# Kernel tuning notes

Hardware: AMD Instinct MI355X
Metric: run time of the kernel (lower is better)

## Reference

```python
import jax, jax.numpy as jnp
import numpy as np

N, E, T, F_IN, D, H, C, OUT = 50000, 500000, 8, 128, 256, 32, 8, 64
EPS = 1e-5


def setup_inputs() -> dict:
    key = jax.random.key(0)
    ks = jax.random.split(key, 20)
    p = lambda k, shp, s=0.05: (jax.random.normal(k, shp, jnp.float32) * s)
    feats = jax.random.normal(ks[0], (T, N, F_IN), jnp.float32)
    edge_index = jax.random.randint(ks[1], (T, 2, E), 0, N)
    return dict(
        feats=feats, edge_index=edge_index,
        W1=p(ks[2], (D, F_IN)), a_s1=p(ks[3], (H, C)), a_d1=p(ks[4], (H, C)), b1=jnp.zeros((D,), jnp.float32),
        W2=p(ks[5], (D, D)), a_s2=p(ks[6], (H, C)), a_d2=p(ks[7], (H, C)), b2=jnp.zeros((D,), jnp.float32),
        ln_g=jnp.ones((D,), jnp.float32), ln_b=jnp.zeros((D,), jnp.float32),
        Wqkv=p(ks[8], (3 * D, D)), bqkv=jnp.zeros((3 * D,), jnp.float32),
        Wo=p(ks[9], (D, D)), bo=jnp.zeros((D,), jnp.float32),
        Wout=p(ks[10], (OUT, D)), bout=jnp.zeros((OUT,), jnp.float32),
        bn_g=jnp.ones((OUT,), jnp.float32), bn_b=jnp.zeros((OUT,), jnp.float32),
    )


def _gat(x, src, dst, W, a_s, a_d, b):
    # PyG GATConv: proj -> per-edge logits -> LeakyReLU(0.2) -> segment softmax over dst -> scatter-add
    h = (x @ W.T).reshape(N, H, C)                       # [N,H,C]
    es = (h * a_s).sum(-1)                               # [N,H]
    ed = (h * a_d).sum(-1)
    e = jax.nn.leaky_relu(es[src] + ed[dst], 0.2)        # [Etot,H]
    m = jax.ops.segment_max(e, dst, num_segments=N)
    ex = jnp.exp(e - m[dst])
    denom = jax.ops.segment_sum(ex, dst, num_segments=N)
    alpha = ex / denom[dst]                              # [Etot,H]
    out = jax.ops.segment_sum(alpha[:, :, None] * h[src], dst, num_segments=N)
    return out.reshape(N, D) + b


def _forward(feats, edge_index, W1, a_s1, a_d1, b1, W2, a_s2, a_d2, b2,
             ln_g, ln_b, Wqkv, bqkv, Wo, bo, Wout, bout, bn_g, bn_b):
    loops = jnp.broadcast_to(jnp.arange(N), (T, N))
    src_all = jnp.concatenate([edge_index[:, 0, :], loops], axis=1)  # self-loops (PyG default)
    dst_all = jnp.concatenate([edge_index[:, 1, :], loops], axis=1)

    def step(_, xs):
        x, src, dst = xs
        x = _gat(x, src, dst, W1, a_s1, a_d1, b1)
        x = _gat(x, src, dst, W2, a_s2, a_d2, b2)
        mu = x.mean(-1, keepdims=True)
        v = x.var(-1, keepdims=True)
        x = (x - mu) / jnp.sqrt(v + EPS) * ln_g + ln_b   # LayerNorm
        return None, jax.nn.relu(x)

    _, emb = jax.lax.scan(step, None, (feats, src_all, dst_all))     # [T,N,D]

    # temporal MHA (seq=T, batch=N, 1 head)
    Wq, Wk, Wv = jnp.split(Wqkv, 3, axis=0)
    bq, bk, bv = jnp.split(bqkv, 3, axis=0)
    q = emb @ Wq.T + bq
    k = emb @ Wk.T + bk
    v = emb @ Wv.T + bv
    scores = jnp.einsum('tnd,snd->nts', q, k) / jnp.sqrt(jnp.float32(D))
    w = jax.nn.softmax(scores, axis=-1)
    attn = jnp.einsum('nts,snd->tnd', w, v)
    o = attn @ Wo.T + bo

    last = o[-1]                                          # [N,D]
    logits = last @ Wout.T + bout                         # [N,OUT]
    mu = logits.mean(0)
    var = logits.var(0)                                   # biased, as in BN training
    y = (logits - mu) / jnp.sqrt(var + EPS) * bn_g + bn_b
    return jax.nn.log_softmax(y, axis=1)


def reference(feats, edge_index, W1, a_s1, a_d1, b1, W2, a_s2, a_d2, b2,
              ln_g, ln_b, Wqkv, bqkv, Wo, bo, Wout, bout, bn_g, bn_b):
    return _forward(feats, edge_index, W1, a_s1, a_d1, b1, W2, a_s2, a_d2, b2,
                    ln_g, ln_b, Wqkv, bqkv, Wo, bo, Wout, bout, bn_g, bn_b)
```

## Files before the change

kernel.cpp:

```cpp
#include <hip/hip_runtime.h>
#include <cstdint>
#include <cstddef>

#define Nn 50000
#define Ee 500000
#define ETOT (Ee + Nn)
#define Tt 8
#define FIN 128
#define Dd 256
#define Hh 32
#define Cc 8
#define OUTC 64
#define EPSC 1e-5f
#define G1 49

typedef __attribute__((ext_vector_type(8))) short bfrag;
typedef __attribute__((ext_vector_type(4))) float ffrag;

static __device__ __forceinline__ unsigned short f2bf(float f) {
    unsigned u = __builtin_bit_cast(unsigned, f);
    u += 0x7fffu + ((u >> 16) & 1u);
    return (unsigned short)(u >> 16);
}
static __device__ __forceinline__ float bf2f(unsigned short h) {
    unsigned u = ((unsigned)h) << 16;
    return __builtin_bit_cast(float, u);
}

__global__ void k_cast(const float* __restrict__ s, unsigned short* __restrict__ d, long n4)
{
    long i = (long)blockIdx.x * 256 + threadIdx.x;
    long stride = (long)gridDim.x * 256;
    for (; i < n4; i += stride) {
        float4 v = ((const float4*)s)[i];
        ushort4 o;
        o.x = f2bf(v.x); o.y = f2bf(v.y); o.z = f2bf(v.z); o.w = f2bf(v.w);
        ((ushort4*)d)[i] = o;
    }
}

__global__ void k_bmat(const float* __restrict__ Wqkv, const float* __restrict__ bqkv,
                       float* __restrict__ BmatT, float* __restrict__ bqk)
{
    int gid = blockIdx.x * 256 + threadIdx.x;
    if (gid < Dd * Dd) {
        int j = gid >> 8, k = gid & 255;
        float s = 0.f;
        for (int r = 0; r < Dd; ++r)
            s += Wqkv[r * Dd + k] * Wqkv[(Dd + r) * Dd + j];
        BmatT[j * Dd + k] = s;
    } else if (gid < Dd * Dd + Dd) {
        int j = gid - Dd * Dd;
        float s = 0.f;
        for (int r = 0; r < Dd; ++r)
            s += bqkv[r] * Wqkv[(Dd + r) * Dd + j];
        bqk[j] = s;
    }
}

__global__ void k_wowv(const float* __restrict__ Wo, const float* __restrict__ Wqkv,
                       const float* __restrict__ bqkv, const float* __restrict__ bo,
                       float* __restrict__ WoWv, float* __restrict__ tmpv)
{
    int gid = blockIdx.x * 256 + threadIdx.x;
    if (gid < Dd * Dd) {
        int i = gid >> 8, j = gid & 255;
        float s = 0.f;
        for (int r = 0; r < Dd; ++r)
            s += Wo[i * Dd + r] * Wqkv[(2 * Dd + r) * Dd + j];
        WoWv[i * Dd + j] = s;
    } else if (gid < Dd * Dd + Dd) {
        int i = gid - Dd * Dd;
        float s = 0.f;
        for (int r = 0; r < Dd; ++r)
            s += Wo[i * Dd + r] * bqkv[2 * Dd + r];
        tmpv[i] = s + bo[i];
    }
}

__global__ void k_mcomb(const float* __restrict__ Wout, const float* __restrict__ WoWv,
                        const float* __restrict__ tmpv, const float* __restrict__ bout,
                        float* __restrict__ Mc, float* __restrict__ cvec)
{
    int gid = blockIdx.x * 256 + threadIdx.x;
    if (gid < OUTC * Dd) {
        int o = gid >> 8, j = gid & 255;
        float s = 0.f;
        for (int i = 0; i < Dd; ++i)
            s += Wout[o * Dd + i] * WoWv[i * Dd + j];
        Mc[o * Dd + j] = s;
    } else if (gid < OUTC * Dd + OUTC) {
        int o = gid - OUTC * Dd;
        float s = 0.f;
        for (int i = 0; i < Dd; ++i)
            s += Wout[o * Dd + i] * tmpv[i];
        cvec[o] = s + bout[o];
    }
}

__global__ void k_foldB(const float* __restrict__ W, const float* __restrict__ a_s,
                        const float* __restrict__ a_d, unsigned short* __restrict__ Baug, int K)
{
    int gid = blockIdx.x * 256 + threadIdx.x;
    if (gid >= 320 * K) return;
    int n = gid / K, k = gid - n * K;
    float v;
    if (n < 256) {
        v = W[n * K + k];
    } else if (n < 288) {
        int hh = n - 256; v = 0.f;
        #pragma unroll
        for (int c = 0; c < 8; ++c) v += a_s[hh * 8 + c] * W[(hh * 8 + c) * K + k];
    } else {
        int hh = n - 288; v = 0.f;
        #pragma unroll
        for (int c = 0; c < 8; ++c) v += a_d[hh * 8 + c] * W[(hh * 8 + c) * K + k];
    }
    Baug[gid] = f2bf(v);
}

__global__ void k_deg_all(const int* __restrict__ eidx, int* __restrict__ deg)
{
    int t = blockIdx.y;
    int e = blockIdx.x * 256 + threadIdx.x;
    if (e >= ETOT) return;
    const int* dstp = eidx + (size_t)t * 2 * Ee + Ee;
    int d = (e < Ee) ? dstp[e] : (e - Ee);
    atomicAdd(&deg[(size_t)t * Nn + d], 1);
}

__global__ void k_scan1(const int* __restrict__ deg, int* __restrict__ part)
{
    int t = blockIdx.y, b = blockIdx.x, tid = threadIdx.x;
    const int* dp = deg + (size_t)t * Nn;
    int base = b * 1024 + tid * 4;
    int s = 0;
    #pragma unroll
    for (int j = 0; j < 4; ++j) { int i = base + j; if (i < Nn) s += dp[i]; }
    __shared__ int red[256];
    red[tid] = s; __syncthreads();
    for (int off = 128; off > 0; off >>= 1) {
        if (tid < off) red[tid] += red[tid + off];
        __syncthreads();
    }
    if (tid == 0) part[t * G1 + b] = red[0];
}

__global__ void k_scan2(int* __restrict__ part, int* __restrict__ rowp)
{
    int t = blockIdx.x, lane = threadIdx.x;
    int v = (lane < G1) ? part[t * G1 + lane] : 0;
    int s = v;
    #pragma unroll
    for (int off = 1; off < 64; off <<= 1) {
        int x = __shfl_up(s, off);
        if (lane >= off) s += x;
    }
    if (lane < G1) part[t * G1 + lane] = s - v;
    if (lane == G1 - 1) rowp[(size_t)t * (Nn + 1) + Nn] = s;
}

__global__ void k_scan3(const int* __restrict__ deg, const int* __restrict__ part,
                        int* __restrict__ rowp, int* __restrict__ wp)
{
    int t = blockIdx.y, b = blockIdx.x, tid = threadIdx.x;
    const int* dp = deg + (size_t)t * Nn;
    int base = b * 1024 + tid * 4;
    int v[4]; int s = 0;
    #pragma unroll
    for (int j = 0; j < 4; ++j) {
        v[j] = (base + j < Nn) ? dp[base + j] : 0;
        s += v[j];
    }
    __shared__ int sc[256];
    sc[tid] = s; __syncthreads();
    for (int off = 1; off < 256; off <<= 1) {
        int x = (tid >= off) ? sc[tid - off] : 0;
        __syncthreads();
        sc[tid] += x;
        __syncthreads();
    }
    int run = part[t * G1 + b] + (sc[tid] - s);
    int* rp = rowp + (size_t)t * (Nn + 1);
    int* wpp = wp + (size_t)t * Nn;
    #pragma unroll
    for (int j = 0; j < 4; ++j) {
        if (base + j < Nn) { rp[base + j] = run; wpp[base + j] = run; run += v[j]; }
    }
}

__global__ void k_fill_all(const int* __restrict__ eidx, int* __restrict__ wp,
                           unsigned short* __restrict__ elist)
{
    int t = blockIdx.y;
    int e = blockIdx.x * 256 + threadIdx.x;
    if (e >= ETOT) return;
    const int* srcp = eidx + (size_t)t * 2 * Ee;
    const int* dstp = srcp + Ee;
    int s, d;
    if (e < Ee) { s = srcp[e]; d = dstp[e]; }
    else        { s = e - Ee;  d = s; }
    int pos = atomicAdd(&wp[(size_t)t * Nn + d], 1);
    elist[(size_t)t * ETOT + pos] = (unsigned short)s;
}

template<int K, int N, bool OUT_BF16, bool A_FP32, bool ESED>
__global__ __launch_bounds__(256, 2) void k_gemm2(
    const void* __restrict__ Av, const unsigned short* __restrict__ B,
    const float* __restrict__ bias, void* __restrict__ Cv, int M,
    unsigned short* __restrict__ es, unsigned short* __restrict__ ed)
{
    constexpr int KC = 128;
    constexpr int KH = K / KC;
    constexpr int KSH = KC / 32;
    constexpr int NSUB = N / 16;
    constexpr int NSUB_C = ESED ? 16 : NSUB;
    constexpr int CST = ESED ? 256 : N;

    __shared__ unsigned short Bs[N * KC];

    const int tid = threadIdx.x;
    const int wave = tid >> 6, lane = tid & 63;
    const int col = lane & 15, quad = lane >> 4;
    const int tile0 = blockIdx.x * 8 + wave * 2;

    const int r0 = tile0 * 16 + col;
    const int r1 = r0 + 16;
    const int r0c = (r0 < M) ? r0 : (M - 1);
    const int r1c = (r1 < M) ? r1 : (M - 1);

    ffrag acc[2][NSUB];
    #pragma unroll
    for (int rt = 0; rt < 2; ++rt)
        #pragma unroll
        for (int ns = 0; ns < NSUB; ++ns) acc[rt][ns] = ffrag{0.f, 0.f, 0.f, 0.f};

    #pragma unroll
    for (int kh = 0; kh < KH; ++kh) {
        if (kh) __syncthreads();
        {
            int rest = wave;
            #pragma unroll
            for (int it = 0; it < N / 16; ++it, rest += 4) {
                int ns  = rest >> 2;
                int ksl = rest & 3;
                const unsigned short* gp =
                    B + (size_t)(ns * 16 + col) * K + kh * KC + ksl * 32 + quad * 8;
                __builtin_amdgcn_global_load_lds(
                    (const __attribute__((address_space(1))) void*)gp,
                    (__attribute__((address_space(3))) void*)(Bs + rest * 512),
                    16, 0, 0);
            }
        }
        __syncthreads();

        bfrag af[2][KSH];
        if (A_FP32) {
            const float* a0 = (const float*)Av + (size_t)r0c * K + kh * KC + quad * 8;
            const float* a1 = (const float*)Av + (size_t)r1c * K + kh * KC + quad * 8;
            #pragma unroll
            for (int ks = 0; ks < KSH; ++ks) {
                float4 x0 = *(const float4*)(a0 + ks * 32);
                float4 x1 = *(const float4*)(a0 + ks * 32 + 4);
                float4 y0 = *(const float4*)(a1 + ks * 32);
                float4 y1 = *(const float4*)(a1 + ks * 32 + 4);
                bfrag f0, f1;
                f0[0] = (short)f2bf(x0.x); f0[1] = (short)f2bf(x0.y);
                f0[2] = (short)f2bf(x0.z); f0[3] = (short)f2bf(x0.w);
                f0[4] = (short)f2bf(x1.x); f0[5] = (short)f2bf(x1.y);
                f0[6] = (short)f2bf(x1.z); f0[7] = (short)f2bf(x1.w);
                f1[0] = (short)f2bf(y0.x); f1[1] = (short)f2bf(y0.y);
                f1[2] = (short)f2bf(y0.z); f1[3] = (short)f2bf(y0.w);
                f1[4] = (short)f2bf(y1.x); f1[5] = (short)f2bf(y1.y);
                f1[6] = (short)f2bf(y1.z); f1[7] = (short)f2bf(y1.w);
                af[0][ks] = f0; af[1][ks] = f1;
            }
        } else {
            const unsigned short* a0 = (const unsigned short*)Av + (size_t)r0c * K + kh * KC + quad * 8;
            const unsigned short* a1 = (const unsigned short*)Av + (size_t)r1c * K + kh * KC + quad * 8;
            #pragma unroll
            for (int ks = 0; ks < KSH; ++ks) {
                af[0][ks] = *(const bfrag*)(a0 + ks * 32);
                af[1][ks] = *(const bfrag*)(a1 + ks * 32);
            }
        }

        const unsigned short* bsl = &Bs[quad * 128 + col * 8];
        #pragma unroll
        for (int ns = 0; ns < NSUB; ++ns) {
            #pragma unroll
            for (int ksl = 0; ksl < KSH; ++ksl) {
                bfrag bf = *(const bfrag*)(bsl + (size_t)(ns * KSH + ksl) * 512);
                acc[0][ns] = __builtin_amdgcn_mfma_f32_16x16x32_bf16(af[0][ksl], bf, acc[0][ns], 0, 0, 0);
                acc[1][ns] = __builtin_amdgcn_mfma_f32_16x16x32_bf16(af[1][ksl], bf, acc[1][ns], 0, 0, 0);
            }
        }
    }

    #pragma unroll
    for (int rt = 0; rt < 2; ++rt) {
        int m0 = (tile0 + rt) * 16;
        #pragma unroll
        for (int ns = 0; ns < NSUB_C; ++ns) {
            float bv = bias ? bias[ns * 16 + col] : 0.f;
            #pragma unroll
            for (int r = 0; r < 4; ++r) {
                int m = m0 + quad * 4 + r;
                if (m < M) {
                    float v = acc[rt][ns][r] + bv;
                    if (OUT_BF16)
                        ((unsigned short*)Cv)[(size_t)m * CST + ns * 16 + col] = f2bf(v);
                    else
                        ((float*)Cv)[(size_t)m * CST + ns * 16 + col] = v;
                }
            }
        }
        if (ESED) {
            #pragma unroll
            for (int ns = 16; ns < 20; ++ns) {
                unsigned short* dst = (ns < 18) ? es : ed;
                int hh = (ns & 1) * 16 + col;
                #pragma unroll
                for (int r = 0; r < 4; ++r) {
                    int m = m0 + quad * 4 + r;
                    if (m < M) dst[(size_t)m * Hh + hh] = f2bf(acc[rt][ns][r]);
                }
            }
        }
    }
}

template<bool DO_LN>
__global__ __launch_bounds__(256) void k_agg(
    const unsigned short* __restrict__ h, const unsigned short* __restrict__ es,
    const unsigned short* __restrict__ ed,
    const int* __restrict__ rowp, const unsigned short* __restrict__ elist,
    const float* __restrict__ bvec, const float* __restrict__ lng, const float* __restrict__ lnb,
    unsigned short* __restrict__ outp)
{
    int wave = threadIdx.x >> 6, lane = threadIdx.x & 63;
    int half = lane >> 5, lh = lane & 31;
    int t = blockIdx.y;
    int n = blockIdx.x * 4 + wave;
    size_t row = (size_t)t * Nn + n;
    const int* rp = rowp + (size_t)t * (Nn + 1);
    const unsigned short* el = elist + (size_t)t * ETOT;
    const size_t tbase = (size_t)t * Nn;

    float edv = bf2f(ed[row * Hh + lh]);
    int r0 = rp[n], r1 = rp[n + 1];
    float den = 0.f;
    float acc[8] = {};
    #pragma unroll 2
    for (int i = r0 + half; i < r1; i += 2) {
        int s = el[i];
        float x = bf2f(es[(tbase + s) * Hh + lh]) + edv;
        x = fmaxf(x, 0.2f * x);
        float p = __expf(x);
        den += p;
        bfrag hv = *(const bfrag*)(h + (tbase + s) * Dd + lh * Cc);
        #pragma unroll
        for (int c = 0; c < 8; ++c) acc[c] += p * bf2f((unsigned short)hv[c]);
    }
    den += __shfl_xor(den, 32);
    #pragma unroll
    for (int c = 0; c < 8; ++c) acc[c] += __shfl_xor(acc[c], 32);

    float inv = 1.0f / den;
    float4 bv0 = *(const float4*)(bvec + lh * Cc);
    float4 bv1 = *(const float4*)(bvec + lh * Cc + 4);
    float o[8];
    o[0] = acc[0] * inv + bv0.x; o[1] = acc[1] * inv + bv0.y;
    o[2] = acc[2] * inv + bv0.z; o[3] = acc[3] * inv + bv0.w;
    o[4] = acc[4] * inv + bv1.x; o[5] = acc[5] * inv + bv1.y;
    o[6] = acc[6] * inv + bv1.z; o[7] = acc[7] * inv + bv1.w;

    if (DO_LN) {
        float s1 = 0.f, s2 = 0.f;
        #pragma unroll
        for (int c = 0; c < 8; ++c) { s1 += o[c]; s2 += o[c] * o[c]; }
        #pragma unroll
        for (int off = 16; off > 0; off >>= 1) {
            s1 += __shfl_xor(s1, off);
            s2 += __shfl_xor(s2, off);
        }
        float mu = s1 * (1.0f / Dd);
        float var = s2 * (1.0f / Dd) - mu * mu;
        float rstd = rsqrtf(var + EPSC);
        float4 g0 = *(const float4*)(lng + lh * Cc);
        float4 g1 = *(const float4*)(lng + lh * Cc + 4);
        float4 l0 = *(const float4*)(lnb + lh * Cc);
        float4 l1 = *(const float4*)(lnb + lh * Cc + 4);
        float gg[8] = {g0.x, g0.y, g0.z, g0.w, g1.x, g1.y, g1.z, g1.w};
        float ll[8] = {l0.x, l0.y, l0.z, l0.w, l1.x, l1.y, l1.z, l1.w};
        #pragma unroll
        for (int c = 0; c < 8; ++c)
            o[c] = fmaxf((o[c] - mu) * rstd * gg[c] + ll[c], 0.f);
    }
    if (half == 0) {
        bfrag ob;
        #pragma unroll
        for (int c = 0; c < 8; ++c) ob[c] = (short)f2bf(o[c]);
        *(bfrag*)(outp + row * Dd + lh * Cc) = ob;
    }
}

__global__ __launch_bounds__(256) void k_attn(const unsigned short* __restrict__ emb,
                                              const unsigned short* __restrict__ qt,
                                              unsigned short* __restrict__ z)
{
    int wave = threadIdx.x >> 6, lane = threadIdx.x & 63;
    int half = lane >> 5, lh = lane & 31;
    int n = blockIdx.x * 8 + wave * 2 + half;
    if (n >= Nn) return;
    bfrag qv = *(const bfrag*)(qt + (size_t)n * Dd + lh * 8);
    float q[8];
    #pragma unroll
    for (int c = 0; c < 8; ++c) q[c] = bf2f((unsigned short)qv[c]);
    bfrag ev[Tt];
    float sc[Tt];
    #pragma unroll
    for (int s = 0; s < Tt; ++s) {
        ev[s] = *(const bfrag*)(emb + ((size_t)s * Nn + n) * Dd + lh * 8);
        float d = 0.f;
        #pragma unroll
        for (int c = 0; c < 8; ++c) d += q[c] * bf2f((unsigned short)ev[s][c]);
        sc[s] = d;
    }
    #pragma unroll
    for (int off = 16; off > 0; off >>= 1)
        #pragma unroll
        for (int s = 0; s < Tt; ++s) sc[s] += __shfl_xor(sc[s], off);
    float mx = -3.0e38f;
    #pragma unroll
    for (int s = 0; s < Tt; ++s) { sc[s] *= 0.0625f; mx = fmaxf(mx, sc[s]); }
    float w[Tt], den = 0.f;
    #pragma unroll
    for (int s = 0; s < Tt; ++s) { w[s] = __expf(sc[s] - mx); den += w[s]; }
    float inv = 1.0f / den;
    float zc[8] = {};
    #pragma unroll
    for (int s = 0; s < Tt; ++s) {
        float ws = w[s] * inv;
        #pragma unroll
        for (int c = 0; c < 8; ++c) zc[c] += ws * bf2f((unsigned short)ev[s][c]);
    }
    bfrag ob;
    #pragma unroll
    for (int c = 0; c < 8; ++c) ob[c] = (short)f2bf(zc[c]);
    *(bfrag*)(z + (size_t)n * Dd + lh * 8) = ob;
}

__global__ __launch_bounds__(256) void k_bnstat(const float* __restrict__ logits,
                                                float* __restrict__ bsum, float* __restrict__ bsq)
{
    __shared__ float ls[256], lq[256];
    int t = threadIdx.x;
    int ch = t & 63;
    float s = 0.f, q = 0.f;
    for (int row = blockIdx.x * 4 + (t >> 6); row < Nn; row += gridDim.x * 4) {
        float v = logits[(size_t)row * OUTC + ch];
        s += v; q += v * v;
    }
    ls[t] = s; lq[t] = q;
    __syncthreads();
    if (t < 64) {
        s = ls[t] + ls[t + 64] + ls[t + 128] + ls[t + 192];
        q = lq[t] + lq[t + 64] + lq[t + 128] + lq[t + 192];
        atomicAdd(&bsum[t], s);
        atomicAdd(&bsq[t], q);
    }
}

__global__ __launch_bounds__(256) void k_final(const float* __restrict__ logits,
                                               const float* __restrict__ bsum, const float* __restrict__ bsq,
                                               const float* __restrict__ g, const float* __restrict__ b,
                                               float* __restrict__ outp)
{
    int lane = threadIdx.x & 63;
    int row = blockIdx.x * 4 + (threadIdx.x >> 6);
    if (row >= Nn) return;
    float v = logits[(size_t)row * OUTC + lane];
    float mu = bsum[lane] * (1.0f / Nn);
    float var = bsq[lane] * (1.0f / Nn) - mu * mu;
    float y = (v - mu) * rsqrtf(var + EPSC) * g[lane] + b[lane];
    float mx = y;
    #pragma unroll
    for (int off = 32; off > 0; off >>= 1) mx = fmaxf(mx, __shfl_xor(mx, off));
    float ex = __expf(y - mx);
    float den = ex;
    #pragma unroll
    for (int off = 32; off > 0; off >>= 1) den += __shfl_xor(den, off);
    outp[(size_t)row * OUTC + lane] = y - mx - __logf(den);
}

extern "C" void kernel_launch(void* const* d_in, const int* in_sizes, int n_in,
                              void* d_out, int out_size, void* d_ws, size_t ws_size,
                              hipStream_t stream)
{
    const float* feats = (const float*)d_in[0];
    const int*   eidx  = (const int*)d_in[1];
    const float* W1    = (const float*)d_in[2];
    const float* a_s1  = (const float*)d_in[3];
    const float* a_d1  = (const float*)d_in[4];
    const float* b1    = (const float*)d_in[5];
    const float* W2    = (const float*)d_in[6];
    const float* a_s2  = (const float*)d_in[7];
    const float* a_d2  = (const float*)d_in[8];
    const float* b2    = (const float*)d_in[9];
    const float* ln_g  = (const float*)d_in[10];
    const float* ln_b  = (const float*)d_in[11];
    const float* Wqkv  = (const float*)d_in[12];
    const float* bqkv  = (const float*)d_in[13];
    const float* Wo    = (const float*)d_in[14];
    const float* bo    = (const float*)d_in[15];
    const float* Wout  = (const float*)d_in[16];
    const float* bout  = (const float*)d_in[17];
    const float* bn_g  = (const float*)d_in[18];
    const float* bn_b  = (const float*)d_in[19];
    float* outp = (float*)d_out;

    char* p = (char*)d_ws;
    auto alloc = [&](size_t bytes) -> void* {
        void* r = (void*)p;
        p += (bytes + 255) & ~(size_t)255;
        return r;
    };
    unsigned short* embb  = (unsigned short*)alloc((size_t)Tt * Nn * Dd * 2);
    unsigned short* hball = (unsigned short*)alloc((size_t)Tt * Nn * Dd * 2);
    unsigned short* xball = (unsigned short*)alloc((size_t)Tt * Nn * Dd * 2);
    unsigned short* es    = (unsigned short*)alloc((size_t)Tt * Nn * Hh * 2);
    unsigned short* ed    = (unsigned short*)alloc((size_t)Tt * Nn * Hh * 2);
    float* logits = (float*)alloc((size_t)Nn * OUTC * 4);
    int*   deg    = (int*)alloc((size_t)Tt * Nn * 4);
    int*   rowp   = (int*)alloc((size_t)Tt * (Nn + 1) * 4);
    int*   wp     = (int*)alloc((size_t)Tt * Nn * 4);
    unsigned short* elist = (unsigned short*)alloc((size_t)Tt * ETOT * 2);
    int*   part   = (int*)alloc((size_t)Tt * G1 * 4);
    float* BmatT  = (float*)alloc((size_t)Dd * Dd * 4);
    float* bqk    = (float*)alloc((size_t)Dd * 4);
    float* WoWv   = (float*)alloc((size_t)Dd * Dd * 4);
    float* Mc     = (float*)alloc((size_t)OUTC * Dd * 4);
    float* tmpv   = (float*)alloc((size_t)Dd * 4);
    float* cvec   = (float*)alloc((size_t)OUTC * 4);
    float* bsum   = (float*)alloc((size_t)OUTC * 4);
    float* bsq    = (float*)alloc((size_t)OUTC * 4);
    unsigned short* Baug1  = (unsigned short*)alloc((size_t)320 * FIN * 2);
    unsigned short* Baug2  = (unsigned short*)alloc((size_t)320 * Dd * 2);
    unsigned short* BmatTb = (unsigned short*)alloc((size_t)Dd * Dd * 2);
    unsigned short* Mcb    = (unsigned short*)alloc((size_t)OUTC * Dd * 2);

    k_bmat<<<(Dd * Dd + Dd + 255) / 256, 256, 0, stream>>>(Wqkv, bqkv, BmatT, bqk);
    k_wowv<<<(Dd * Dd + Dd + 255) / 256, 256, 0, stream>>>(Wo, Wqkv, bqkv, bo, WoWv, tmpv);
    k_mcomb<<<(OUTC * Dd + OUTC + 255) / 256, 256, 0, stream>>>(Wout, WoWv, tmpv, bout, Mc, cvec);
    k_foldB<<<(320 * FIN + 255) / 256, 256, 0, stream>>>(W1, a_s1, a_d1, Baug1, FIN);
    k_foldB<<<(320 * Dd + 255) / 256, 256, 0, stream>>>(W2, a_s2, a_d2, Baug2, Dd);
    k_cast<<<(Dd * Dd / 4 + 255) / 256, 256, 0, stream>>>(BmatT, BmatTb, Dd * Dd / 4);
    k_cast<<<(OUTC * Dd / 4 + 255) / 256, 256, 0, stream>>>(Mc, Mcb, OUTC * Dd / 4);

    hipMemsetAsync(deg, 0, (size_t)Tt * Nn * 4, stream);
    k_deg_all<<<dim3((ETOT + 255) / 256, Tt), 256, 0, stream>>>(eidx, deg);
    k_scan1<<<dim3(G1, Tt), 256, 0, stream>>>(deg, part);
    k_scan2<<<Tt, 64, 0, stream>>>(part, rowp);
    k_scan3<<<dim3(G1, Tt), 256, 0, stream>>>(deg, part, rowp, wp);
    k_fill_all<<<dim3((ETOT + 255) / 256, Tt), 256, 0, stream>>>(eidx, wp, elist);

    const int MALL = Tt * Nn;
    const int gridAll = MALL / 128;
    const int gridOne = (Nn / 16 + 7) / 8;

    k_gemm2<FIN, 320, true, true, true><<<gridAll, 256, 0, stream>>>(
        feats, Baug1, nullptr, hball, MALL, es, ed);
    k_agg<false><<<dim3(Nn / 4, Tt), 256, 0, stream>>>(
        hball, es, ed, rowp, elist, b1, nullptr, nullptr, xball);
    k_gemm2<Dd, 320, true, false, true><<<gridAll, 256, 0, stream>>>(
        xball, Baug2, nullptr, hball, MALL, es, ed);
    k_agg<true><<<dim3(Nn / 4, Tt), 256, 0, stream>>>(
        hball, es, ed, rowp, elist, b2, ln_g, ln_b, embb);

    k_gemm2<Dd, Dd, true, false, false><<<gridOne, 256, 0, stream>>>(
        embb + (size_t)(Tt - 1) * Nn * Dd, BmatTb, bqk, hball, Nn, nullptr, nullptr);
    k_attn<<<(Nn + 7) / 8, 256, 0, stream>>>(embb, hball, xball);
    k_gemm2<Dd, OUTC, false, false, false><<<gridOne, 256, 0, stream>>>(
        xball, Mcb, cvec, logits, Nn, nullptr, nullptr);

    hipMemsetAsync(bsum, 0, OUTC * 4, stream);
    hipMemsetAsync(bsq, 0, OUTC * 4, stream);
    k_bnstat<<<256, 256, 0, stream>>>(logits, bsum, bsq);
    k_final<<<Nn / 4, 256, 0, stream>>>(logits, bsum, bsq, bn_g, bn_b, outp);
}
```

Measured before the change: 2.046 ms.

## Compute GAT attention logits in aggregation instead of augmented GEMM columns

Removes the folded a_s/a_d columns from the projection GEMM (320 to 256 outputs) and the separate es/ed buffers. The aggregation kernel now computes each edge's source logit as a dot product of the gathered bf16 features with a_s, and the destination logit from the node's own row. This cuts GEMM work and the es/ed writes and gathers, but adds 8 FMAs per edge per lane in the gather loop and computes logits from bf16-rounded features.

```diff
diff --git a/kernel.cpp b/kernel.cpp
--- a/kernel.cpp
+++ b/kernel.cpp
@@ -98,27 +98,6 @@
     }
 }
 
-__global__ void k_foldB(const float* __restrict__ W, const float* __restrict__ a_s,
-                        const float* __restrict__ a_d, unsigned short* __restrict__ Baug, int K)
-{
-    int gid = blockIdx.x * 256 + threadIdx.x;
-    if (gid >= 320 * K) return;
-    int n = gid / K, k = gid - n * K;
-    float v;
-    if (n < 256) {
-        v = W[n * K + k];
-    } else if (n < 288) {
-        int hh = n - 256; v = 0.f;
-        #pragma unroll
-        for (int c = 0; c < 8; ++c) v += a_s[hh * 8 + c] * W[(hh * 8 + c) * K + k];
-    } else {
-        int hh = n - 288; v = 0.f;
-        #pragma unroll
-        for (int c = 0; c < 8; ++c) v += a_d[hh * 8 + c] * W[(hh * 8 + c) * K + k];
-    }
-    Baug[gid] = f2bf(v);
-}
-
 __global__ void k_deg_all(const int* __restrict__ eidx, int* __restrict__ deg)
 {
     int t = blockIdx.y;
@@ -204,18 +183,15 @@
     elist[(size_t)t * ETOT + pos] = (unsigned short)s;
 }
 
-template<int K, int N, bool OUT_BF16, bool A_FP32, bool ESED>
+template<int K, int N, bool OUT_BF16, bool A_FP32>
 __global__ __launch_bounds__(256, 2) void k_gemm2(
     const void* __restrict__ Av, const unsigned short* __restrict__ B,
-    const float* __restrict__ bias, void* __restrict__ Cv, int M,
-    unsigned short* __restrict__ es, unsigned short* __restrict__ ed)
+    const float* __restrict__ bias, void* __restrict__ Cv, int M)
 {
     constexpr int KC = 128;
     constexpr int KH = K / KC;
     constexpr int KSH = KC / 32;
     constexpr int NSUB = N / 16;
-    constexpr int NSUB_C = ESED ? 16 : NSUB;
-    constexpr int CST = ESED ? 256 : N;
 
     __shared__ unsigned short Bs[N * KC];
 
@@ -301,7 +277,7 @@
     for (int rt = 0; rt < 2; ++rt) {
         int m0 = (tile0 + rt) * 16;
         #pragma unroll
-        for (int ns = 0; ns < NSUB_C; ++ns) {
+        for (int ns = 0; ns < NSUB; ++ns) {
             float bv = bias ? bias[ns * 16 + col] : 0.f;
             #pragma unroll
             for (int r = 0; r < 4; ++r) {
@@ -309,31 +285,19 @@
                 if (m < M) {
                     float v = acc[rt][ns][r] + bv;
                     if (OUT_BF16)
-                        ((unsigned short*)Cv)[(size_t)m * CST + ns * 16 + col] = f2bf(v);
+                        ((unsigned short*)Cv)[(size_t)m * N + ns * 16 + col] = f2bf(v);
                     else
-                        ((float*)Cv)[(size_t)m * CST + ns * 16 + col] = v;
+                        ((float*)Cv)[(size_t)m * N + ns * 16 + col] = v;
                 }
             }
         }
-        if (ESED) {
-            #pragma unroll
-            for (int ns = 16; ns < 20; ++ns) {
-                unsigned short* dst = (ns < 18) ? es : ed;
-                int hh = (ns & 1) * 16 + col;
-                #pragma unroll
-                for (int r = 0; r < 4; ++r) {
-                    int m = m0 + quad * 4 + r;
-                    if (m < M) dst[(size_t)m * Hh + hh] = f2bf(acc[rt][ns][r]);
-                }
-            }
-        }
     }
 }
 
 template<bool DO_LN>
 __global__ __launch_bounds__(256) void k_agg(
-    const unsigned short* __restrict__ h, const unsigned short* __restrict__ es,
-    const unsigned short* __restrict__ ed,
+    const unsigned short* __restrict__ h,
+    const float* __restrict__ a_s, const float* __restrict__ a_d,
     const int* __restrict__ rowp, const unsigned short* __restrict__ elist,
     const float* __restrict__ bvec, const float* __restrict__ lng, const float* __restrict__ lnb,
     unsigned short* __restrict__ outp)
@@ -347,20 +311,36 @@
     const unsigned short* el = elist + (size_t)t * ETOT;
     const size_t tbase = (size_t)t * Nn;
 
-    float edv = bf2f(ed[row * Hh + lh]);
+    float4 as0 = *(const float4*)(a_s + lh * Cc);
+    float4 as1 = *(const float4*)(a_s + lh * Cc + 4);
+    float4 ad0 = *(const float4*)(a_d + lh * Cc);
+    float4 ad1 = *(const float4*)(a_d + lh * Cc + 4);
+    float as_[8] = {as0.x, as0.y, as0.z, as0.w, as1.x, as1.y, as1.z, as1.w};
+
+    bfrag hn = *(const bfrag*)(h + row * Dd + lh * Cc);
+    float edv = ad0.x * bf2f((unsigned short)hn[0]) + ad0.y * bf2f((unsigned short)hn[1])
+              + ad0.z * bf2f((unsigned short)hn[2]) + ad0.w * bf2f((unsigned short)hn[3])
+              + ad1.x * bf2f((unsigned short)hn[4]) + ad1.y * bf2f((unsigned short)hn[5])
+              + ad1.z * bf2f((unsigned short)hn[6]) + ad1.w * bf2f((unsigned short)hn[7]);
+
     int r0 = rp[n], r1 = rp[n + 1];
     float den = 0.f;
     float acc[8] = {};
     #pragma unroll 2
     for (int i = r0 + half; i < r1; i += 2) {
         int s = el[i];
-        float x = bf2f(es[(tbase + s) * Hh + lh]) + edv;
+        bfrag hv = *(const bfrag*)(h + (tbase + s) * Dd + lh * Cc);
+        float hc[8];
+        #pragma unroll
+        for (int c = 0; c < 8; ++c) hc[c] = bf2f((unsigned short)hv[c]);
+        float x = edv;
+        #pragma unroll
+        for (int c = 0; c < 8; ++c) x += as_[c] * hc[c];
         x = fmaxf(x, 0.2f * x);
         float p = __expf(x);
         den += p;
-        bfrag hv = *(const bfrag*)(h + (tbase + s) * Dd + lh * Cc);
-        #pragma unroll
-        for (int c = 0; c < 8; ++c) acc[c] += p * bf2f((unsigned short)hv[c]);
+        #pragma unroll
+        for (int c = 0; c < 8; ++c) acc[c] += p * hc[c];
     }
     den += __shfl_xor(den, 32);
     #pragma unroll
@@ -529,8 +509,6 @@
     unsigned short* embb  = (unsigned short*)alloc((size_t)Tt * Nn * Dd * 2);
     unsigned short* hball = (unsigned short*)alloc((size_t)Tt * Nn * Dd * 2);
     unsigned short* xball = (unsigned short*)alloc((size_t)Tt * Nn * Dd * 2);
-    unsigned short* es    = (unsigned short*)alloc((size_t)Tt * Nn * Hh * 2);
-    unsigned short* ed    = (unsigned short*)alloc((size_t)Tt * Nn * Hh * 2);
     float* logits = (float*)alloc((size_t)Nn * OUTC * 4);
     int*   deg    = (int*)alloc((size_t)Tt * Nn * 4);
     int*   rowp   = (int*)alloc((size_t)Tt * (Nn + 1) * 4);
@@ -545,16 +523,16 @@
     float* cvec   = (float*)alloc((size_t)OUTC * 4);
     float* bsum   = (float*)alloc((size_t)OUTC * 4);
     float* bsq    = (float*)alloc((size_t)OUTC * 4);
-    unsigned short* Baug1  = (unsigned short*)alloc((size_t)320 * FIN * 2);
-    unsigned short* Baug2  = (unsigned short*)alloc((size_t)320 * Dd * 2);
+    unsigned short* Wb1    = (unsigned short*)alloc((size_t)Dd * FIN * 2);
+    unsigned short* Wb2    = (unsigned short*)alloc((size_t)Dd * Dd * 2);
     unsigned short* BmatTb = (unsigned short*)alloc((size_t)Dd * Dd * 2);
     unsigned short* Mcb    = (unsigned short*)alloc((size_t)OUTC * Dd * 2);
 
     k_bmat<<<(Dd * Dd + Dd + 255) / 256, 256, 0, stream>>>(Wqkv, bqkv, BmatT, bqk);
     k_wowv<<<(Dd * Dd + Dd + 255) / 256, 256, 0, stream>>>(Wo, Wqkv, bqkv, bo, WoWv, tmpv);
     k_mcomb<<<(OUTC * Dd + OUTC + 255) / 256, 256, 0, stream>>>(Wout, WoWv, tmpv, bout, Mc, cvec);
-    k_foldB<<<(320 * FIN + 255) / 256, 256, 0, stream>>>(W1, a_s1, a_d1, Baug1, FIN);
-    k_foldB<<<(320 * Dd + 255) / 256, 256, 0, stream>>>(W2, a_s2, a_d2, Baug2, Dd);
+    k_cast<<<(Dd * FIN / 4 + 255) / 256, 256, 0, stream>>>(W1, Wb1, Dd * FIN / 4);
+    k_cast<<<(Dd * Dd / 4 + 255) / 256, 256, 0, stream>>>(W2, Wb2, Dd * Dd / 4);
     k_cast<<<(Dd * Dd / 4 + 255) / 256, 256, 0, stream>>>(BmatT, BmatTb, Dd * Dd / 4);
     k_cast<<<(OUTC * Dd / 4 + 255) / 256, 256, 0, stream>>>(Mc, Mcb, OUTC * Dd / 4);
 
@@ -569,20 +547,20 @@
     const int gridAll = MALL / 128;
     const int gridOne = (Nn / 16 + 7) / 8;
 
-    k_gemm2<FIN, 320, true, true, true><<<gridAll, 256, 0, stream>>>(
-        feats, Baug1, nullptr, hball, MALL, es, ed);
+    k_gemm2<FIN, Dd, true, true><<<gridAll, 256, 0, stream>>>(
+        feats, Wb1, nullptr, hball, MALL);
     k_agg<false><<<dim3(Nn / 4, Tt), 256, 0, stream>>>(
-        hball, es, ed, rowp, elist, b1, nullptr, nullptr, xball);
-    k_gemm2<Dd, 320, true, false, true><<<gridAll, 256, 0, stream>>>(
-        xball, Baug2, nullptr, hball, MALL, es, ed);
+        hball, a_s1, a_d1, rowp, elist, b1, nullptr, nullptr, xball);
+    k_gemm2<Dd, Dd, true, false><<<gridAll, 256, 0, stream>>>(
+        xball, Wb2, nullptr, hball, MALL);
     k_agg<true><<<dim3(Nn / 4, Tt), 256, 0, stream>>>(
-        hball, es, ed, rowp, elist, b2, ln_g, ln_b, embb);
-
-    k_gemm2<Dd, Dd, true, false, false><<<gridOne, 256, 0, stream>>>(
-        embb + (size_t)(Tt - 1) * Nn * Dd, BmatTb, bqk, hball, Nn, nullptr, nullptr);
+        hball, a_s2, a_d2, rowp, elist, b2, ln_g, ln_b, embb);
+
+    k_gemm2<Dd, Dd, true, false><<<gridOne, 256, 0, stream>>>(
+        embb + (size_t)(Tt - 1) * Nn * Dd, BmatTb, bqk, hball, Nn);
     k_attn<<<(Nn + 7) / 8, 256, 0, stream>>>(embb, hball, xball);
-    k_gemm2<Dd, OUTC, false, false, false><<<gridOne, 256, 0, stream>>>(
-        xball, Mcb, cvec, logits, Nn, nullptr, nullptr);
+    k_gemm2<Dd, OUTC, false, false><<<gridOne, 256, 0, stream>>>(
+        xball, Mcb, cvec, logits, Nn);
 
     hipMemsetAsync(bsum, 0, OUTC * 4, stream);
     hipMemsetAsync(bsq, 0, OUTC * 4, stream);
```

Measured after the change: 1.890 ms. 7.6% less time.
